# Kernel tuning notes

Hardware: AMD Instinct MI355X
Metric: run time of the kernel (lower is better)

## Reference

```python
import jax, jax.numpy as jnp
import numpy as np


def _next_pow2(n: int) -> int:
    # matches torch: 2 ** ceil(log2(n))
    return 1 << (int(n) - 1).bit_length()


def setup_inputs() -> dict:
    key = jax.random.key(0)
    k1, k2 = jax.random.split(key)
    B, T, L = 256, 32768, 32768
    x = jax.random.normal(k1, (B, T), dtype=jnp.float32)
    filt = jax.random.normal(k2, (1, L), dtype=jnp.float32)
    return {"x": x, "filt": filt}


def reference(x, filt):
    """EpochedFutureFill.forward: exact causal convolution of x with filt.

    The per-token epoched algorithm (tau-step direct sum + FutureFill FFT
    cache refresh every K steps, cache initialized to zero) computes exactly
    y[b, t] = sum_{s=0}^{min(t, L-1)} filt[0, s] * x[b, t-s].
    We compute it with one FFT-based linear convolution, mirroring the
    float32 FFT math of future_fill().
    """
    B, T = x.shape
    L = filt.shape[-1]
    n_fft = _next_pow2(T + L - 1)
    xf = jnp.fft.rfft(x.astype(jnp.float32), n=n_fft)          # (B, n_fft//2+1)
    wf = jnp.fft.rfft(filt.astype(jnp.float32), n=n_fft)       # (1, n_fft//2+1)
    y = jnp.fft.irfft(xf * wf, n=n_fft)[:, :T]                 # causal lags 0..T-1
    return y.astype(x.dtype)
```

## Files before the change

kernel.cpp:

```cpp
#include <hip/hip_runtime.h>
#include <cstdint>

typedef __attribute__((ext_vector_type(8))) short short8;
typedef __attribute__((ext_vector_type(4))) float floatx4;

#define TWO_PI 6.283185307179586f

__device__ __forceinline__ unsigned short f2bf(float f) {
  union { float f; uint32_t u; } c; c.f = f;
  uint32_t u = c.u;
  u += 0x7FFFu + ((u >> 16) & 1u);
  return (unsigned short)(u >> 16);
}
__device__ __forceinline__ uint32_t packbf(float re, float im) {
  return (uint32_t)f2bf(re) | ((uint32_t)f2bf(im) << 16);
}


__global__ __launch_bounds__(256) void prep_all(
    const float* __restrict__ x, const float* __restrict__ filt,
    unsigned short* __restrict__ A1, unsigned short* __restrict__ A2,
    unsigned short* __restrict__ A3, unsigned short* __restrict__ A4,
    uint32_t* __restrict__ Zp, float2* __restrict__ Gw,
    float2* __restrict__ Tw) {
  const int bid = blockIdx.x;
  const int tid = threadIdx.x;
  const float w256 = TWO_PI / 256.0f;
  if (bid < 3072) {
    int idx = bid * 256 + tid;
    if (idx < 131072) {
      int col = idx & 255, row = idx >> 8;
      int k1 = row >> 1, d = row & 1, r = col >> 1, e = col & 1;
      float th = (float)((k1 * r) & 255) * w256;
      float sn, cs; __sincosf(th, &sn, &cs);
      A1[idx] = f2bf(d == 0 ? (e == 0 ? cs : sn) : (e == 0 ? -sn : cs));
    } else if (idx < 393216) {
      int j = idx - 131072;
      int col = j & 511, row = j >> 9;
      int k2 = row >> 1, d = row & 1, cc = col >> 1, e = col & 1;
      float th = (float)((k2 * cc) & 255) * w256;
      float sn, cs; __sincosf(th, &sn, &cs);
      A2[j] = f2bf(d == 0 ? (e == 0 ? cs : sn) : (e == 0 ? -sn : cs));
    } else if (idx < 655360) {
      int j = idx - 393216;
      int col = j & 511, row = j >> 9;
      int cc = row >> 1, d = row & 1, k2 = col >> 1, e = col & 1;
      float th = (float)((k2 * cc) & 255) * w256;
      float sn, cs; __sincosf(th, &sn, &cs);
      A3[j] = f2bf(d == 0 ? (e == 0 ? cs : -sn) : (e == 0 ? sn : cs));
    } else {
      int j = idx - 655360;
      int col = j & 511, row = j >> 9;
      int r = row >> 1, d = row & 1, k1 = col >> 1, e = col & 1;
      float th = (float)((k1 * r) & 255) * w256;
      float sn, cs; __sincosf(th, &sn, &cs);
      A4[j] = f2bf(d == 0 ? (e == 0 ? cs : -sn) : (e == 0 ? sn : cs));
    }
  } else if (bid < 4096) {
    int b2 = bid - 3072;
    int s = b2 >> 3, rq = b2 & 7;
    const float* x0 = x + (size_t)(2 * s) * 32768;
    const float* x1 = x0 + 32768;
    uint32_t v[16];
    #pragma unroll
    for (int rr = 0; rr < 16; ++rr) {
      int t = tid + 256 * (rq * 16 + rr);
      v[rr] = (uint32_t)f2bf(x0[t]) | ((uint32_t)f2bf(x1[t]) << 16);
    }
    uint32_t* dst = Zp + (size_t)(s * 256 + tid) * 128 + rq * 16;
    #pragma unroll
    for (int j = 0; j < 16; j += 4)
      *(uint4*)(dst + j) = make_uint4(v[j], v[j + 1], v[j + 2], v[j + 3]);
  } else if (bid < 4352) {
    int k1 = bid - 4096, c = tid;
    float ar = 0.f, ai = 0.f;
    for (int r = 0; r < 128; ++r) {
      float v = filt[c + 256 * r];
      float th = (float)((k1 * r) & 255) * w256;
      float sn, cs; __sincosf(th, &sn, &cs);
      ar += v * cs; ai -= v * sn;
    }
    float th = (float)((k1 * c) & 65535) * (TWO_PI / 65536.0f);
    float sn, cs; __sincosf(th, &sn, &cs);
    Gw[(k1 << 8) + c] = make_float2(ar * cs + ai * sn, ai * cs - ar * sn);
  } else {
    int k1 = bid - 4352, c = tid;
    float th = (float)((k1 * c) & 65535) * (TWO_PI / 65536.0f);
    float sn, cs; __sincosf(th, &sn, &cs);
    Tw[(k1 << 8) + c] = make_float2(cs, sn);
  }
}

__global__ __launch_bounds__(256) void prep_wb(const float2* __restrict__ Gw,
                                               float2* __restrict__ WtT) {
  int k1 = blockIdx.x, k2 = threadIdx.x;
  float ar = 0.f, ai = 0.f;
  for (int c = 0; c < 256; ++c) {
    float2 g = Gw[(k1 << 8) + c];
    float th = (float)((k2 * c) & 255) * (TWO_PI / 256.0f);
    float sn, cs; __sincosf(th, &sn, &cs);
    ar += g.x * cs + g.y * sn;
    ai += g.y * cs - g.x * sn;
  }
  WtT[(k2 << 8) + k1] = make_float2(ar, ai);
}

template <int MODE, int NCHUNK>
__global__ __launch_bounds__(256, 2) void dft_stage(
    const unsigned short* __restrict__ Af,
    const unsigned short* __restrict__ Bd,
    uint32_t* __restrict__ outp,
    float* __restrict__ yout,
    const float2* __restrict__ tab) {
  __shared__ unsigned short Sm[32768];
  constexpr int KP = NCHUNK * 32;

  const int mt = blockIdx.x >> 8;
  const int nt = blockIdx.x & 255;
  const int m0 = mt * 128, n0 = nt * 128;

  const int tid = threadIdx.x;
  const int w = tid >> 6, lane = tid & 63;
  const int qlo = lane & 15, qhi = lane >> 4;
  const int wr = w >> 1, wc = w & 1;
  const int lj = lane >> 3;
  const int g = (lane & 7) ^ lj;
  const int hsel = g & 1, qk8 = (g >> 1) << 3;

  floatx4 acc[4][4];
  #pragma unroll
  for (int i = 0; i < 4; ++i)
    #pragma unroll
    for (int j = 0; j < 4; ++j) acc[i][j] = (floatx4){0.f, 0.f, 0.f, 0.f};

  auto issue = [&](int t) {
    const int buf = t & 3;
    const int k0 = t * 32;
    unsigned short* Asb = Sm + buf * 4096;
    unsigned short* Bsb = Sm + 16384 + buf * 4096;
    #pragma unroll
    for (int q = 0; q < 2; ++q) {
      const int PL = w * 16 + q * 8;
      const int R = 2 * (PL + lj) + hsel;
      const unsigned short* gA = Af + (size_t)(m0 + R) * KP + k0 + qk8;
      const unsigned short* gB = Bd + (size_t)(n0 + R) * KP + k0 + qk8;
      __builtin_amdgcn_global_load_lds(
          (const __attribute__((address_space(1))) uint32_t*)gA,
          (__attribute__((address_space(3))) uint32_t*)&Asb[PL * 64], 16, 0, 0);
      __builtin_amdgcn_global_load_lds(
          (const __attribute__((address_space(1))) uint32_t*)gB,
          (__attribute__((address_space(3))) uint32_t*)&Bsb[PL * 64], 16, 0, 0);
    }
  };

  issue(0); issue(1); issue(2);
  #pragma unroll
  for (int t = 0; t < NCHUNK; ++t) {
    const int rem = NCHUNK - 1 - t;
    if (rem >= 2)      asm volatile("s_waitcnt vmcnt(8)" ::: "memory");
    else if (rem == 1) asm volatile("s_waitcnt vmcnt(4)" ::: "memory");
    else               asm volatile("s_waitcnt vmcnt(0)" ::: "memory");
    __builtin_amdgcn_s_barrier();
    if (t + 3 < NCHUNK) issue(t + 3);
    __builtin_amdgcn_sched_barrier(0);
    const unsigned short* Ab = Sm + (t & 3) * 4096;
    const unsigned short* Bb = Sm + 16384 + (t & 3) * 4096;
    short8 a[4], bb[4];
    #pragma unroll
    for (int im = 0; im < 4; ++im) {
      const int R = wr * 64 + im * 16 + qlo;
      const int P = R >> 1;
      a[im] = *(const short8*)&Ab[(P << 6) + ((((qhi << 1) | (R & 1)) ^ (P & 7)) << 3)];
    }
    #pragma unroll
    for (int in = 0; in < 4; ++in) {
      const int R = wc * 64 + in * 16 + qlo;
      const int P = R >> 1;
      bb[in] = *(const short8*)&Bb[(P << 6) + ((((qhi << 1) | (R & 1)) ^ (P & 7)) << 3)];
    }
    __builtin_amdgcn_s_setprio(1);
    #pragma unroll
    for (int im = 0; im < 4; ++im)
      #pragma unroll
      for (int in = 0; in < 4; ++in)
        acc[im][in] = __builtin_amdgcn_mfma_f32_16x16x32_bf16(a[im], bb[in], acc[im][in], 0, 0, 0);
    __builtin_amdgcn_s_setprio(0);
  }

  const int s_idx = n0 >> 8;
  const int cl0 = n0 & 255;

  if (MODE == 2) {
    __syncthreads();
    uint32_t* Tr = (uint32_t*)Sm;
    #pragma unroll
    for (int im = 0; im < 4; ++im) {
      const int mloc = wr * 32 + im * 8 + qhi * 2;
      #pragma unroll
      for (int in = 0; in < 4; ++in) {
        const int nloc = wc * 64 + in * 16 + qlo;
        #pragma unroll
        for (int pp = 0; pp < 2; ++pp) {
          const int mC = (m0 >> 1) + mloc + pp;
          float re = acc[im][in][2 * pp], iv = acc[im][in][2 * pp + 1];
          float2 wv = tab[(mC << 8) + cl0 + nloc];
          float r2 = re * wv.x - iv * wv.y, i2 = re * wv.y + iv * wv.x;
          Tr[nloc * 68 + mloc + pp] = packbf(r2, i2);
        }
      }
    }
    __syncthreads();
    const int ln = tid >> 1, half = tid & 1;
    uint32_t* dst = outp + (size_t)((s_idx << 8) + cl0 + ln) * 256 + (m0 >> 1) + half * 32;
    const uint32_t* srcp = Tr + ln * 68 + half * 32;
    #pragma unroll
    for (int j = 0; j < 32; j += 4)
      *(uint4*)(dst + j) = *(const uint4*)(srcp + j);
    return;
  }

  #pragma unroll
  for (int im = 0; im < 4; ++im) {
    const int mloc = wr * 32 + im * 8 + qhi * 2;
    #pragma unroll
    for (int in = 0; in < 4; ++in) {
      const int nloc = wc * 64 + in * 16 + qlo;
      const int cloc = cl0 + nloc;
      #pragma unroll
      for (int pp = 0; pp < 2; ++pp) {
        const int mC = (m0 >> 1) + mloc + pp;
        float re = acc[im][in][2 * pp], iv = acc[im][in][2 * pp + 1];
        if (MODE == 1) {
          float2 tw = tab[(mC << 8) + cloc];
          float r2 = re * tw.x + iv * tw.y, i2 = iv * tw.x - re * tw.y;
          outp[(size_t)((s_idx << 8) + mC) * 256 + cloc] = packbf(r2, i2);
        } else if (MODE == 3) {
          float2 tw = tab[(mC << 8) + cloc];
          float r2 = re * tw.x - iv * tw.y, i2 = iv * tw.x + re * tw.y;
          outp[(size_t)((s_idx << 8) + mC) * 256 + cloc] = packbf(r2, i2);
        } else {
          const float sc = 1.0f / 65536.0f;
          float* y0 = yout + ((size_t)s_idx << 16) + (mC << 8) + cloc;
          y0[0] = re * sc;
          y0[32768] = iv * sc;
        }
      }
    }
  }
}

extern "C" void kernel_launch(void* const* d_in, const int* in_sizes, int n_in,
                              void* d_out, int out_size, void* d_ws, size_t ws_size,
                              hipStream_t stream) {
  const float* x = (const float*)d_in[0];
  const float* filt = (const float*)d_in[1];
  float* Y = (float*)d_out;

  char* ws = (char*)d_ws;
  unsigned short* A1 = (unsigned short*)(ws + 0);
  unsigned short* A2 = (unsigned short*)(ws + 0x40000);
  unsigned short* A3 = (unsigned short*)(ws + 0xC0000);
  unsigned short* A4 = (unsigned short*)(ws + 0x140000);
  float2* Gw  = (float2*)(ws + 0x180000);
  float2* WtT = (float2*)(ws + 0x200000);
  float2* Tw  = (float2*)(ws + 0x280000);
  unsigned short* Zp = (unsigned short*)(ws + (3u << 20));
  unsigned short* G2 = (unsigned short*)(ws + 19922944u);
  unsigned short* P  = (unsigned short*)(ws + 53477376u);
  unsigned short* H2 = (unsigned short*)(ws + (3u << 20));

  hipLaunchKernelGGL(prep_all, dim3(4608), dim3(256), 0, stream,
                     x, filt, A1, A2, A3, A4, (uint32_t*)Zp, Gw, Tw);
  hipLaunchKernelGGL(prep_wb, dim3(256), dim3(256), 0, stream, Gw, WtT);

  hipLaunchKernelGGL((dft_stage<1, 8>), dim3(1024), dim3(256), 0, stream,
                     A1, Zp, (uint32_t*)G2, (float*)nullptr, Tw);
  hipLaunchKernelGGL((dft_stage<2, 16>), dim3(1024), dim3(256), 0, stream,
                     A2, G2, (uint32_t*)P, (float*)nullptr, WtT);
  hipLaunchKernelGGL((dft_stage<3, 16>), dim3(1024), dim3(256), 0, stream,
                     A3, P, (uint32_t*)H2, (float*)nullptr, Tw);
  hipLaunchKernelGGL((dft_stage<4, 16>), dim3(512), dim3(256), 0, stream,
                     A4, H2, (uint32_t*)nullptr, Y, Tw);
}
```

Before: 205.9 us.

## Halve LDS to double-buffered tiles for four blocks per CU

Reduces the shared-memory staging in the DFT GEMM stage from a 4-deep to a 2-deep ring. That halves LDS use so launch bounds can request four resident blocks per CU instead of two. The global-to-LDS load layout and swizzle are reworked into a simpler row-major 32-element layout with an XOR slot swizzle. The MODE 2 transpose epilogue is split into two halves so it fits in the smaller LDS buffer. In exchange, prefetch depth drops to one chunk with a full vmcnt(0) wait every iteration, and 4 blocks per CU caps registers per thread, which could cause spills with 64 accumulator floats.

```diff
diff --git a/kernel.cpp b/kernel.cpp
--- a/kernel.cpp
+++ b/kernel.cpp
@@ -106,13 +106,13 @@
 }
 
 template <int MODE, int NCHUNK>
-__global__ __launch_bounds__(256, 2) void dft_stage(
+__global__ __launch_bounds__(256, 4) void dft_stage(
     const unsigned short* __restrict__ Af,
     const unsigned short* __restrict__ Bd,
     uint32_t* __restrict__ outp,
     float* __restrict__ yout,
     const float2* __restrict__ tab) {
-  __shared__ unsigned short Sm[32768];
+  __shared__ unsigned short Sm[16384];
   constexpr int KP = NCHUNK * 32;
 
   const int mt = blockIdx.x >> 8;
@@ -123,9 +123,8 @@
   const int w = tid >> 6, lane = tid & 63;
   const int qlo = lane & 15, qhi = lane >> 4;
   const int wr = w >> 1, wc = w & 1;
-  const int lj = lane >> 3;
-  const int g = (lane & 7) ^ lj;
-  const int hsel = g & 1, qk8 = (g >> 1) << 3;
+  const int rsub = lane >> 2;
+  const int koff = ((lane & 3) ^ ((lane >> 3) & 3)) << 3;
 
   floatx4 acc[4][4];
   #pragma unroll
@@ -134,49 +133,46 @@
     for (int j = 0; j < 4; ++j) acc[i][j] = (floatx4){0.f, 0.f, 0.f, 0.f};
 
   auto issue = [&](int t) {
-    const int buf = t & 3;
+    const int buf = t & 1;
     const int k0 = t * 32;
     unsigned short* Asb = Sm + buf * 4096;
-    unsigned short* Bsb = Sm + 16384 + buf * 4096;
+    unsigned short* Bsb = Sm + 8192 + buf * 4096;
     #pragma unroll
     for (int q = 0; q < 2; ++q) {
-      const int PL = w * 16 + q * 8;
-      const int R = 2 * (PL + lj) + hsel;
-      const unsigned short* gA = Af + (size_t)(m0 + R) * KP + k0 + qk8;
-      const unsigned short* gB = Bd + (size_t)(n0 + R) * KP + k0 + qk8;
+      const int rowbase = w * 32 + q * 16;
+      const int R = rowbase + rsub;
+      const unsigned short* gA = Af + (size_t)(m0 + R) * KP + k0 + koff;
+      const unsigned short* gB = Bd + (size_t)(n0 + R) * KP + k0 + koff;
       __builtin_amdgcn_global_load_lds(
           (const __attribute__((address_space(1))) uint32_t*)gA,
-          (__attribute__((address_space(3))) uint32_t*)&Asb[PL * 64], 16, 0, 0);
+          (__attribute__((address_space(3))) uint32_t*)&Asb[rowbase * 32], 16, 0, 0);
       __builtin_amdgcn_global_load_lds(
           (const __attribute__((address_space(1))) uint32_t*)gB,
-          (__attribute__((address_space(3))) uint32_t*)&Bsb[PL * 64], 16, 0, 0);
+          (__attribute__((address_space(3))) uint32_t*)&Bsb[rowbase * 32], 16, 0, 0);
     }
   };
 
-  issue(0); issue(1); issue(2);
+  issue(0);
   #pragma unroll
   for (int t = 0; t < NCHUNK; ++t) {
-    const int rem = NCHUNK - 1 - t;
-    if (rem >= 2)      asm volatile("s_waitcnt vmcnt(8)" ::: "memory");
-    else if (rem == 1) asm volatile("s_waitcnt vmcnt(4)" ::: "memory");
-    else               asm volatile("s_waitcnt vmcnt(0)" ::: "memory");
+    asm volatile("s_waitcnt vmcnt(0)" ::: "memory");
     __builtin_amdgcn_s_barrier();
-    if (t + 3 < NCHUNK) issue(t + 3);
+    if (t + 1 < NCHUNK) issue(t + 1);
     __builtin_amdgcn_sched_barrier(0);
-    const unsigned short* Ab = Sm + (t & 3) * 4096;
-    const unsigned short* Bb = Sm + 16384 + (t & 3) * 4096;
+    const unsigned short* Ab = Sm + (t & 1) * 4096;
+    const unsigned short* Bb = Sm + 8192 + (t & 1) * 4096;
     short8 a[4], bb[4];
     #pragma unroll
     for (int im = 0; im < 4; ++im) {
       const int R = wr * 64 + im * 16 + qlo;
-      const int P = R >> 1;
-      a[im] = *(const short8*)&Ab[(P << 6) + ((((qhi << 1) | (R & 1)) ^ (P & 7)) << 3)];
+      const int slot = qhi ^ ((R >> 1) & 3);
+      a[im] = *(const short8*)&Ab[R * 32 + slot * 8];
     }
     #pragma unroll
     for (int in = 0; in < 4; ++in) {
       const int R = wc * 64 + in * 16 + qlo;
-      const int P = R >> 1;
-      bb[in] = *(const short8*)&Bb[(P << 6) + ((((qhi << 1) | (R & 1)) ^ (P & 7)) << 3)];
+      const int slot = qhi ^ ((R >> 1) & 3);
+      bb[in] = *(const short8*)&Bb[R * 32 + slot * 8];
     }
     __builtin_amdgcn_s_setprio(1);
     #pragma unroll
@@ -191,31 +187,37 @@
   const int cl0 = n0 & 255;
 
   if (MODE == 2) {
-    __syncthreads();
     uint32_t* Tr = (uint32_t*)Sm;
     #pragma unroll
-    for (int im = 0; im < 4; ++im) {
-      const int mloc = wr * 32 + im * 8 + qhi * 2;
-      #pragma unroll
-      for (int in = 0; in < 4; ++in) {
-        const int nloc = wc * 64 + in * 16 + qlo;
+    for (int h = 0; h < 2; ++h) {
+      __syncthreads();
+      if (wc == h) {
         #pragma unroll
-        for (int pp = 0; pp < 2; ++pp) {
-          const int mC = (m0 >> 1) + mloc + pp;
-          float re = acc[im][in][2 * pp], iv = acc[im][in][2 * pp + 1];
-          float2 wv = tab[(mC << 8) + cl0 + nloc];
-          float r2 = re * wv.x - iv * wv.y, i2 = re * wv.y + iv * wv.x;
-          Tr[nloc * 68 + mloc + pp] = packbf(r2, i2);
+        for (int im = 0; im < 4; ++im) {
+          const int mloc = wr * 32 + im * 8 + qhi * 2;
+          #pragma unroll
+          for (int in = 0; in < 4; ++in) {
+            const int nl = in * 16 + qlo;
+            #pragma unroll
+            for (int pp = 0; pp < 2; ++pp) {
+              const int mC = (m0 >> 1) + mloc + pp;
+              float re = acc[im][in][2 * pp], iv = acc[im][in][2 * pp + 1];
+              float2 wv = tab[(mC << 8) + cl0 + h * 64 + nl];
+              float r2 = re * wv.x - iv * wv.y, i2 = re * wv.y + iv * wv.x;
+              Tr[nl * 68 + mloc + pp] = packbf(r2, i2);
+            }
+          }
         }
       }
-    }
-    __syncthreads();
-    const int ln = tid >> 1, half = tid & 1;
-    uint32_t* dst = outp + (size_t)((s_idx << 8) + cl0 + ln) * 256 + (m0 >> 1) + half * 32;
-    const uint32_t* srcp = Tr + ln * 68 + half * 32;
-    #pragma unroll
-    for (int j = 0; j < 32; j += 4)
-      *(uint4*)(dst + j) = *(const uint4*)(srcp + j);
+      __syncthreads();
+      const int row = tid >> 2, qq = tid & 3;
+      uint32_t* dst = outp + (size_t)((s_idx << 8) + cl0 + h * 64 + row) * 256 +
+                      (m0 >> 1) + qq * 16;
+      const uint32_t* srcp = Tr + row * 68 + qq * 16;
+      #pragma unroll
+      for (int j = 0; j < 16; j += 4)
+        *(uint4*)(dst + j) = *(const uint4*)(srcp + j);
+    }
     return;
   }
 
```

After: 199.8 us. -2.9%, faster.
